# Performance work log

Measured on AMD Instinct MI355X. Metric: run time of the kernel, lower is better.

Reference implementation:

```python
import jax, jax.numpy as jnp
import numpy as np

N_NODES = 100000
N_EDGES = 1600000
N_FEAT = 512
N_HID = 256
N_CLASS = 40


def setup_inputs() -> dict:
    key = jax.random.key(0)
    ks = jax.random.split(key, 6)
    features = jax.random.normal(ks[0], (N_NODES, N_FEAT), dtype=jnp.float32)
    edge_index = jax.random.randint(ks[1], (2, N_EDGES), 0, N_NODES, dtype=jnp.int32)
    edge_weight = jax.random.uniform(ks[2], (N_EDGES,), dtype=jnp.float32)
    # xavier_uniform with gain=1.414 (as in reset_parameters)
    g = 1.414
    lim1 = g * np.sqrt(6.0 / (N_FEAT + N_HID))
    lim2 = g * np.sqrt(6.0 / (N_HID + N_CLASS))
    W1 = jax.random.uniform(ks[3], (N_FEAT, N_HID), minval=-lim1, maxval=lim1, dtype=jnp.float32)
    W2 = jax.random.uniform(ks[4], (N_HID, N_CLASS), minval=-lim2, maxval=lim2, dtype=jnp.float32)
    b1 = jnp.zeros((N_HID,), dtype=jnp.float32)
    b2 = jnp.zeros((N_CLASS,), dtype=jnp.float32)
    return {"features": features, "edge_index": edge_index, "edge_weight": edge_weight,
            "W1": W1, "b1": b1, "W2": W2, "b2": b2}


def _spmm(edge_index, edge_weight, x, n):
    # out[r] = sum over edges e with row[e]==r of w[e] * x[col[e]]
    row, col = edge_index[0], edge_index[1]
    msgs = edge_weight[:, None] * x[col]  # [E, D]
    return jax.ops.segment_sum(msgs, row, num_segments=n)


def reference(features, edge_index, edge_weight, W1, b1, W2, b2):
    n = features.shape[0]
    # Layer 1: linear -> spmm -> relu (dropout is identity in eval mode)
    h = features @ W1 + b1
    h = jax.nn.relu(_spmm(edge_index, edge_weight, h, n))
    # Layer 2: linear -> spmm -> log_softmax
    h = h @ W2 + b2
    h = _spmm(edge_index, edge_weight, h, n)
    return jax.nn.log_softmax(h, axis=1)
```

## Files before the change

kernel.cpp:

```cpp
#include <hip/hip_runtime.h>
#include <stdint.h>

#define N_NODES 100000
#define N_EDGES 1600000
#define N_FEAT 512
#define N_HID 256
#define N_CLASS 40
#define H2SB 64

typedef float f32x4 __attribute__((ext_vector_type(4)));
typedef __bf16 bf16x8 __attribute__((ext_vector_type(8)));
typedef unsigned short u16x4 __attribute__((ext_vector_type(4)));
typedef unsigned short u16x8 __attribute__((ext_vector_type(8)));

__device__ __forceinline__ unsigned short f2bf(float f) {
  unsigned int u = __float_as_uint(f);
  unsigned int r = (u + 0x7FFFu + ((u >> 16) & 1u)) >> 16;
  return (unsigned short)r;
}
__device__ __forceinline__ float bf2f(unsigned short s) {
  return __uint_as_float(((unsigned int)s) << 16);
}
__device__ __forceinline__ float pk_w(unsigned int p) {
  return __uint_as_float((p >> 17) << 16);
}
__device__ __forceinline__ int pk_c(unsigned int p) { return (int)(p & 0x1FFFFu); }

__global__ __launch_bounds__(1024) void k_zero(int* __restrict__ cnt) {
  int i = blockIdx.x * 1024 + threadIdx.x;
  if (i < N_NODES) cnt[i] = 0;
}

#define HIST_BLOCKS 1563
#define W1T_BLOCKS  512
#define W2T_BLOCKS  48
__global__ __launch_bounds__(256) void k_pre(const float* __restrict__ W1,
                                             const float* __restrict__ W2,
                                             const int* __restrict__ ei,
                                             unsigned short* __restrict__ W1t,
                                             unsigned short* __restrict__ W2t,
                                             int* __restrict__ cnt,
                                             int* __restrict__ rank) {
  const int bid = blockIdx.x, tid = threadIdx.x;
  if (bid < HIST_BLOCKS) {
    #pragma unroll
    for (int k = 0; k < 4; ++k) {
      int e = bid * 1024 + k * 256 + tid;
      if (e < N_EDGES) rank[e] = atomicAdd(&cnt[ei[e]], 1);
    }
  } else if (bid < HIST_BLOCKS + W1T_BLOCKS) {
    int gid = (bid - HIST_BLOCKS) * 256 + tid;
    int n = gid >> 9, k = gid & 511;
    W1t[gid] = f2bf(W1[(long)k * N_HID + n]);
  } else {
    int gid = (bid - HIST_BLOCKS - W1T_BLOCKS) * 256 + tid;
    int n = gid >> 8, k = gid & 255;
    W2t[gid] = (n < N_CLASS) ? f2bf(W2[(long)k * N_CLASS + n]) : (unsigned short)0;
  }
}

__global__ __launch_bounds__(1024) void k_scan_a(const int* __restrict__ cnt,
                                                 int* __restrict__ rp,
                                                 int* __restrict__ bsum) {
  __shared__ int sm[1024];
  const int tid = threadIdx.x;
  const int i = blockIdx.x * 1024 + tid;
  int v = (i < N_NODES) ? cnt[i] : 0;
  sm[tid] = v;
  __syncthreads();
  #pragma unroll
  for (int d = 1; d < 1024; d <<= 1) {
    int t = (tid >= d) ? sm[tid - d] : 0;
    __syncthreads();
    sm[tid] += t;
    __syncthreads();
  }
  if (i < N_NODES) rp[i] = sm[tid] - v;
  if (tid == 1023) bsum[blockIdx.x] = sm[1023];
}

__global__ __launch_bounds__(128) void k_scan_b(const int* __restrict__ bsum,
                                                int* __restrict__ boffs,
                                                int* __restrict__ rp) {
  __shared__ int sm[128];
  const int tid = threadIdx.x;
  const int nb = (N_NODES + 1023) >> 10;
  int v = (tid < nb) ? bsum[tid] : 0;
  sm[tid] = v;
  __syncthreads();
  #pragma unroll
  for (int d = 1; d < 128; d <<= 1) {
    int t = (tid >= d) ? sm[tid - d] : 0;
    __syncthreads();
    sm[tid] += t;
    __syncthreads();
  }
  boffs[tid] = sm[tid] - v;
  if (tid == 127) rp[N_NODES] = sm[127];
}

__global__ void k_scan_c(int* __restrict__ rp, const int* __restrict__ boffs) {
  int i = blockIdx.x * 256 + threadIdx.x;
  if (i >= N_NODES) return;
  rp[i] += boffs[i >> 10];
}

#define GEMM_BLOCKS 250
#define SCAT_BLOCKS 782
__global__ __launch_bounds__(1024) void k_fused1(const float* __restrict__ X,
                                                 const unsigned short* __restrict__ W1t,
                                                 const float* __restrict__ b1,
                                                 unsigned short* __restrict__ H1,
                                                 const int* __restrict__ ei,
                                                 const float* __restrict__ ew,
                                                 const int* __restrict__ rank,
                                                 const int* __restrict__ rp,
                                                 unsigned int* __restrict__ cwp) {
  __shared__ __align__(16) unsigned short Bs[128 * 512];
  const int t = threadIdx.x;

  if (blockIdx.x >= GEMM_BLOCKS) {
    int sb = blockIdx.x - GEMM_BLOCKS;
    #pragma unroll
    for (int k = 0; k < 2; ++k) {
      int e = sb * 2048 + k * 1024 + t;
      if (e < N_EDGES) {
        int r = ei[e];
        int pos = rp[r] + rank[e];
        unsigned int w15 = (unsigned int)f2bf(ew[e]);
        cwp[pos] = (w15 << 17) | (unsigned int)ei[N_EDGES + e];
      }
    }
    return;
  }

  const int pair = blockIdx.x >> 1, panel = blockIdx.x & 1;
  const long rb = (long)pair * 800;
  const int n0 = panel * 128;

  {
    const int col = t >> 3, seg = t & 7;
    const unsigned short* src = W1t + (long)(n0 + col) * N_FEAT;
    #pragma unroll
    for (int j = 0; j < 8; ++j) {
      int slot = seg * 8 + j;
      int ps = slot ^ (col & 7);
      *(u16x8*)&Bs[col * 512 + ps * 8] = *(const u16x8*)(src + slot * 8);
    }
  }
  __syncthreads();

  const int lane = t & 63;
  const int wid = t >> 6;
  const int lr = lane & 15;
  const int lkg = lane >> 4;

  for (int c = wid; c < 50; c += 16) {
    const long row0 = rb + c * 16;
    const float* ap = X + (row0 + lr) * N_FEAT + lkg * 8;
    f32x4 acc[8] = {};

    #pragma unroll 2
    for (int k0 = 0; k0 < N_FEAT; k0 += 32) {
      f32x4 xa = __builtin_nontemporal_load((const f32x4*)(ap + k0));
      f32x4 xb = __builtin_nontemporal_load((const f32x4*)(ap + k0 + 4));
      bf16x8 av;
      av[0] = (__bf16)xa[0]; av[1] = (__bf16)xa[1];
      av[2] = (__bf16)xa[2]; av[3] = (__bf16)xa[3];
      av[4] = (__bf16)xb[0]; av[5] = (__bf16)xb[1];
      av[6] = (__bf16)xb[2]; av[7] = (__bf16)xb[3];
      const int slot = (k0 >> 3) + lkg;
      const int ps = slot ^ (lr & 7);
      #pragma unroll
      for (int nt = 0; nt < 8; ++nt) {
        bf16x8 bv = *(const bf16x8*)&Bs[(nt * 16 + lr) * 512 + ps * 8];
        acc[nt] = __builtin_amdgcn_mfma_f32_16x16x32_bf16(av, bv, acc[nt], 0, 0, 0);
      }
    }

    #pragma unroll
    for (int nt = 0; nt < 8; ++nt) {
      int colg = n0 + nt * 16 + lr;
      float bias = b1[colg];
      #pragma unroll
      for (int i = 0; i < 4; ++i) {
        long row = row0 + lkg * 4 + i;
        H1[row * N_HID + colg] = f2bf(acc[nt][i] + bias);
      }
    }
  }
}

__global__ __launch_bounds__(256) void k_spmm1(const int* __restrict__ row_ptr,
                                               const unsigned int* __restrict__ cwp,
                                               const unsigned short* __restrict__ H1,
                                               unsigned short* __restrict__ H1r) {
  int r = blockIdx.x * 4 + (threadIdx.x >> 6);
  int lane = threadIdx.x & 63;
  if (r >= N_NODES) return;
  int s = row_ptr[r], e = row_ptr[r + 1];
  float a0 = 0.f, a1 = 0.f, a2 = 0.f, a3 = 0.f;
  const unsigned short* Hb = H1 + lane * 4;
  int i = s;
  for (; i + 8 <= e; i += 8) {
    uint4 q0 = *(const uint4*)(cwp + i);
    uint4 q1 = *(const uint4*)(cwp + i + 4);
    unsigned int cc[8] = {q0.x, q0.y, q0.z, q0.w, q1.x, q1.y, q1.z, q1.w};
    u16x4 h[8];
    #pragma unroll
    for (int j = 0; j < 8; ++j)
      h[j] = *(const u16x4*)(Hb + (long)pk_c(cc[j]) * N_HID);
    #pragma unroll
    for (int j = 0; j < 8; ++j) {
      float w = pk_w(cc[j]);
      a0 += w * bf2f(h[j][0]);
      a1 += w * bf2f(h[j][1]);
      a2 += w * bf2f(h[j][2]);
      a3 += w * bf2f(h[j][3]);
    }
  }
  for (; i < e; ++i) {
    unsigned int p = cwp[i];
    float w = pk_w(p);
    u16x4 hv = *(const u16x4*)(Hb + (long)pk_c(p) * N_HID);
    a0 += w * bf2f(hv[0]);
    a1 += w * bf2f(hv[1]);
    a2 += w * bf2f(hv[2]);
    a3 += w * bf2f(hv[3]);
  }
  u16x4 o;
  o[0] = f2bf(fmaxf(a0, 0.f));
  o[1] = f2bf(fmaxf(a1, 0.f));
  o[2] = f2bf(fmaxf(a2, 0.f));
  o[3] = f2bf(fmaxf(a3, 0.f));
  *(u16x4*)(H1r + (long)r * N_HID + lane * 4) = o;
}

__global__ __launch_bounds__(256) void k_gemm2(const unsigned short* __restrict__ H1r,
                                               const unsigned short* __restrict__ W2t,
                                               const float* __restrict__ b2,
                                               unsigned short* __restrict__ H2) {
  const int t = threadIdx.x;
  const int lane = t & 63;
  const int wid = t >> 6;
  const long m0 = (long)blockIdx.x * 128;
  const int lr = lane & 15;
  const int lk = (lane >> 4) * 8;

  const unsigned short* Ab[2];
  #pragma unroll
  for (int mt = 0; mt < 2; ++mt) {
    long r = m0 + wid * 32 + mt * 16 + lr;
    if (r >= N_NODES) r = N_NODES - 1;
    Ab[mt] = H1r + r * N_HID + lk;
  }
  const unsigned short* Bb[3];
  #pragma unroll
  for (int nt = 0; nt < 3; ++nt)
    Bb[nt] = W2t + (long)(nt * 16 + lr) * N_HID + lk;

  f32x4 acc[2][3] = {};
  #pragma unroll
  for (int k0 = 0; k0 < N_HID; k0 += 32) {
    bf16x8 av[2], bvv[3];
    #pragma unroll
    for (int mt = 0; mt < 2; ++mt) av[mt] = *(const bf16x8*)(Ab[mt] + k0);
    #pragma unroll
    for (int nt = 0; nt < 3; ++nt) bvv[nt] = *(const bf16x8*)(Bb[nt] + k0);
    #pragma unroll
    for (int mt = 0; mt < 2; ++mt)
      #pragma unroll
      for (int nt = 0; nt < 3; ++nt)
        acc[mt][nt] = __builtin_amdgcn_mfma_f32_16x16x32_bf16(av[mt], bvv[nt], acc[mt][nt], 0, 0, 0);
  }

  #pragma unroll
  for (int nt = 0; nt < 3; ++nt) {
    int col = nt * 16 + lr;
    if (col < N_CLASS) {
      float bias = b2[col];
      #pragma unroll
      for (int mt = 0; mt < 2; ++mt) {
        #pragma unroll
        for (int i = 0; i < 4; ++i) {
          long row = m0 + wid * 32 + mt * 16 + (lane >> 4) * 4 + i;
          if (row < N_NODES) H2[row * H2SB + col] = f2bf(acc[mt][nt][i] + bias);
        }
      }
    }
  }
}

__global__ __launch_bounds__(256) void k_spmm2_lsm(const int* __restrict__ row_ptr,
                                                   const unsigned int* __restrict__ cwp,
                                                   const unsigned short* __restrict__ H2,
                                                   float* __restrict__ out) {
  int r = blockIdx.x * 4 + (threadIdx.x >> 6);
  int lane = threadIdx.x & 63;
  if (r >= N_NODES) return;
  int s = row_ptr[r], e = row_ptr[r + 1];
  float acc = 0.f;
  const bool act = lane < N_CLASS;
  int i = s;
  for (; i + 8 <= e; i += 8) {
    uint4 q0 = *(const uint4*)(cwp + i);
    uint4 q1 = *(const uint4*)(cwp + i + 4);
    unsigned int cc[8] = {q0.x, q0.y, q0.z, q0.w, q1.x, q1.y, q1.z, q1.w};
    float h[8];
    #pragma unroll
    for (int j = 0; j < 8; ++j)
      h[j] = act ? bf2f(H2[(long)pk_c(cc[j]) * H2SB + lane]) : 0.f;
    #pragma unroll
    for (int j = 0; j < 8; ++j) acc += pk_w(cc[j]) * h[j];
  }
  for (; i < e; ++i) {
    unsigned int p = cwp[i];
    if (act) acc += pk_w(p) * bf2f(H2[(long)pk_c(p) * H2SB + lane]);
  }
  float v = act ? acc : -INFINITY;
  float m = v;
  #pragma unroll
  for (int d = 32; d > 0; d >>= 1) m = fmaxf(m, __shfl_xor(m, d));
  float ex = act ? __expf(v - m) : 0.f;
  float ssum = ex;
  #pragma unroll
  for (int d = 32; d > 0; d >>= 1) ssum += __shfl_xor(ssum, d);
  float ls = __logf(ssum);
  if (act) out[(long)r * N_CLASS + lane] = v - m - ls;
}

extern "C" void kernel_launch(void* const* d_in, const int* in_sizes, int n_in,
                              void* d_out, int out_size, void* d_ws, size_t ws_size,
                              hipStream_t stream) {
  (void)in_sizes; (void)n_in; (void)out_size; (void)ws_size;
  const float* X  = (const float*)d_in[0];
  const int*   EI = (const int*)d_in[1];
  const float* EW = (const float*)d_in[2];
  const float* W1 = (const float*)d_in[3];
  const float* b1 = (const float*)d_in[4];
  const float* W2 = (const float*)d_in[5];
  const float* b2 = (const float*)d_in[6];
  float* out = (float*)d_out;

  char* p = (char*)d_ws;
  auto take = [&](size_t bytes) {
    char* r = p;
    p += (bytes + 511) & ~(size_t)511;
    return r;
  };
  unsigned short* W1t   = (unsigned short*)take((size_t)N_HID * N_FEAT * 2);
  unsigned short* W2t   = (unsigned short*)take((size_t)48 * N_HID * 2);
  int*            cnt   = (int*)take((size_t)N_NODES * 4);
  int*            rp    = (int*)take((size_t)(N_NODES + 1) * 4);
  int*            bsum  = (int*)take((size_t)128 * 4);
  int*            boffs = (int*)take((size_t)128 * 4);
  int*            rank  = (int*)take((size_t)N_EDGES * 4);
  unsigned int*   cwp   = (unsigned int*)take((size_t)N_EDGES * 4);
  unsigned short* H1    = (unsigned short*)take((size_t)N_NODES * N_HID * 2);
  unsigned short* H1r   = (unsigned short*)take((size_t)N_NODES * N_HID * 2);
  unsigned short* H2    = (unsigned short*)take((size_t)N_NODES * H2SB * 2);

  const int NB_SCAN = (N_NODES + 1023) / 1024;

  k_zero<<<NB_SCAN, 1024, 0, stream>>>(cnt);
  k_pre<<<HIST_BLOCKS + W1T_BLOCKS + W2T_BLOCKS, 256, 0, stream>>>(W1, W2, EI, W1t, W2t, cnt, rank);
  k_scan_a<<<NB_SCAN, 1024, 0, stream>>>(cnt, rp, bsum);
  k_scan_b<<<1, 128, 0, stream>>>(bsum, boffs, rp);
  k_scan_c<<<(N_NODES + 255) / 256, 256, 0, stream>>>(rp, boffs);
  k_fused1<<<GEMM_BLOCKS + SCAT_BLOCKS, 1024, 0, stream>>>(X, W1t, b1, H1, EI, EW, rank, rp, cwp);
  k_spmm1<<<(N_NODES + 3) / 4, 256, 0, stream>>>(rp, cwp, H1, H1r);
  k_gemm2<<<(N_NODES + 127) / 128, 256, 0, stream>>>(H1r, W2t, b2, H2);
  k_spmm2_lsm<<<(N_NODES + 3) / 4, 256, 0, stream>>>(rp, cwp, H2, out);
}
```

Before: 476.6 us.

## Split fused GEMM1/scatter kernel and store H2 as fp32 with 48 stride

Splits the combined GEMM1 and CSR-scatter kernel into two separate launches: a 512-thread scatter kernel and a 250-block GEMM kernel. This removes the mixed-role grid, where scatter blocks were sized to 1024 threads and carried the large shared-memory allocation. Separately, the layer-2 intermediate H2 is now stored as fp32 with a 48-element row stride instead of bf16 with a 64-element stride. That drops the bf16 rounding and conversion but raises the bytes gathered per edge in the second SpMM. Splitting the kernels also gives up any overlap between the scatter and the GEMM.

```diff
diff --git a/kernel.cpp b/kernel.cpp
--- a/kernel.cpp
+++ b/kernel.cpp
@@ -6,7 +6,7 @@
 #define N_FEAT 512
 #define N_HID 256
 #define N_CLASS 40
-#define H2SB 64
+#define H2S 48
 
 typedef float f32x4 __attribute__((ext_vector_type(4)));
 typedef __bf16 bf16x8 __attribute__((ext_vector_type(8)));
@@ -105,35 +105,30 @@
   rp[i] += boffs[i >> 10];
 }
 
-#define GEMM_BLOCKS 250
-#define SCAT_BLOCKS 782
-__global__ __launch_bounds__(1024) void k_fused1(const float* __restrict__ X,
-                                                 const unsigned short* __restrict__ W1t,
-                                                 const float* __restrict__ b1,
-                                                 unsigned short* __restrict__ H1,
-                                                 const int* __restrict__ ei,
+__global__ __launch_bounds__(512) void k_scatter(const int* __restrict__ ei,
                                                  const float* __restrict__ ew,
                                                  const int* __restrict__ rank,
                                                  const int* __restrict__ rp,
                                                  unsigned int* __restrict__ cwp) {
+  const int t = threadIdx.x;
+  #pragma unroll
+  for (int k = 0; k < 4; ++k) {
+    int e = blockIdx.x * 2048 + k * 512 + t;
+    if (e < N_EDGES) {
+      int r = ei[e];
+      int pos = rp[r] + rank[e];
+      unsigned int w15 = (unsigned int)f2bf(ew[e]);
+      cwp[pos] = (w15 << 17) | (unsigned int)ei[N_EDGES + e];
+    }
+  }
+}
+
+__global__ __launch_bounds__(1024) void k_gemm1(const float* __restrict__ X,
+                                                const unsigned short* __restrict__ W1t,
+                                                const float* __restrict__ b1,
+                                                unsigned short* __restrict__ H1) {
   __shared__ __align__(16) unsigned short Bs[128 * 512];
   const int t = threadIdx.x;
-
-  if (blockIdx.x >= GEMM_BLOCKS) {
-    int sb = blockIdx.x - GEMM_BLOCKS;
-    #pragma unroll
-    for (int k = 0; k < 2; ++k) {
-      int e = sb * 2048 + k * 1024 + t;
-      if (e < N_EDGES) {
-        int r = ei[e];
-        int pos = rp[r] + rank[e];
-        unsigned int w15 = (unsigned int)f2bf(ew[e]);
-        cwp[pos] = (w15 << 17) | (unsigned int)ei[N_EDGES + e];
-      }
-    }
-    return;
-  }
-
   const int pair = blockIdx.x >> 1, panel = blockIdx.x & 1;
   const long rb = (long)pair * 800;
   const int n0 = panel * 128;
@@ -239,7 +234,7 @@
 __global__ __launch_bounds__(256) void k_gemm2(const unsigned short* __restrict__ H1r,
                                                const unsigned short* __restrict__ W2t,
                                                const float* __restrict__ b2,
-                                               unsigned short* __restrict__ H2) {
+                                               float* __restrict__ H2) {
   const int t = threadIdx.x;
   const int lane = t & 63;
   const int wid = t >> 6;
@@ -284,7 +279,7 @@
         #pragma unroll
         for (int i = 0; i < 4; ++i) {
           long row = m0 + wid * 32 + mt * 16 + (lane >> 4) * 4 + i;
-          if (row < N_NODES) H2[row * H2SB + col] = f2bf(acc[mt][nt][i] + bias);
+          if (row < N_NODES) H2[row * H2S + col] = acc[mt][nt][i] + bias;
         }
       }
     }
@@ -293,7 +288,7 @@
 
 __global__ __launch_bounds__(256) void k_spmm2_lsm(const int* __restrict__ row_ptr,
                                                    const unsigned int* __restrict__ cwp,
-                                                   const unsigned short* __restrict__ H2,
+                                                   const float* __restrict__ H2,
                                                    float* __restrict__ out) {
   int r = blockIdx.x * 4 + (threadIdx.x >> 6);
   int lane = threadIdx.x & 63;
@@ -309,13 +304,13 @@
     float h[8];
     #pragma unroll
     for (int j = 0; j < 8; ++j)
-      h[j] = act ? bf2f(H2[(long)pk_c(cc[j]) * H2SB + lane]) : 0.f;
+      h[j] = act ? H2[(long)pk_c(cc[j]) * H2S + lane] : 0.f;
     #pragma unroll
     for (int j = 0; j < 8; ++j) acc += pk_w(cc[j]) * h[j];
   }
   for (; i < e; ++i) {
     unsigned int p = cwp[i];
-    if (act) acc += pk_w(p) * bf2f(H2[(long)pk_c(p) * H2SB + lane]);
+    if (act) acc += pk_w(p) * H2[(long)pk_c(p) * H2S + lane];
   }
   float v = act ? acc : -INFINITY;
   float m = v;
@@ -358,7 +353,7 @@
   unsigned int*   cwp   = (unsigned int*)take((size_t)N_EDGES * 4);
   unsigned short* H1    = (unsigned short*)take((size_t)N_NODES * N_HID * 2);
   unsigned short* H1r   = (unsigned short*)take((size_t)N_NODES * N_HID * 2);
-  unsigned short* H2    = (unsigned short*)take((size_t)N_NODES * H2SB * 2);
+  float*          H2    = (float*)take((size_t)N_NODES * H2S * 4);
 
   const int NB_SCAN = (N_NODES + 1023) / 1024;
 
@@ -367,7 +362,8 @@
   k_scan_a<<<NB_SCAN, 1024, 0, stream>>>(cnt, rp, bsum);
   k_scan_b<<<1, 128, 0, stream>>>(bsum, boffs, rp);
   k_scan_c<<<(N_NODES + 255) / 256, 256, 0, stream>>>(rp, boffs);
-  k_fused1<<<GEMM_BLOCKS + SCAT_BLOCKS, 1024, 0, stream>>>(X, W1t, b1, H1, EI, EW, rank, rp, cwp);
+  k_scatter<<<(N_EDGES + 2047) / 2048, 512, 0, stream>>>(EI, EW, rank, rp, cwp);
+  k_gemm1<<<250, 1024, 0, stream>>>(X, W1t, b1, H1);
   k_spmm1<<<(N_NODES + 3) / 4, 256, 0, stream>>>(rp, cwp, H1, H1r);
   k_gemm2<<<(N_NODES + 127) / 128, 256, 0, stream>>>(H1r, W2t, b2, H2);
   k_spmm2_lsm<<<(N_NODES + 3) / 4, 256, 0, stream>>>(rp, cwp, H2, out);
```

After: 472.6 us. About the same (-0.8%).
